# Performance work log

Measured on AMD Instinct MI355X. Metric: run time of the kernel, lower is better.

The kernel has to match this reference:

```python
import jax, jax.numpy as jnp
import numpy as np

B, K, P = 16, 64, 256
D_MODEL, EXPAND = 512, 2
D_INNER = D_MODEL * EXPAND  # 1024
D_CONV, D_FF, E_LAYERS = 4, 16, 4
DT_RANK = 32  # ceil(512/16)
RANK = 4


def rmsnorm(x, w, eps=1e-5):
    return x * jax.lax.rsqrt(jnp.mean(x * x, axis=-1, keepdims=True) + eps) * w


def selective_scan(u, delta, A, Bm, Cm, Dp):
    # u,delta: [b,l,d]; A: [d,n]; Bm,Cm: [b,l,n]; Dp: [d]
    dA = jnp.exp(jnp.einsum('bld,dn->bldn', delta, A))
    dBu = jnp.einsum('bld,bln,bld->bldn', delta, Bm, u)
    x0 = jnp.zeros((u.shape[0], u.shape[2], A.shape[1]), u.dtype)

    def step(x, t):
        dA_t, dBu_t, c_t = t
        x = dA_t * x + dBu_t
        return x, jnp.einsum('bdn,bn->bd', x, c_t)

    _, ys = jax.lax.scan(step, x0, (dA.swapaxes(0, 1), dBu.swapaxes(0, 1), Cm.swapaxes(0, 1)))
    return ys.swapaxes(0, 1) + u * Dp


def mamba_block(h, in_w, cw, cb, xp_w, dt_w, dt_b, A_log, Dp, out_w):
    b, l, _ = h.shape
    xr = h @ in_w.T  # [b,l,2*d_inner]
    x, res = xr[..., :D_INNER], xr[..., D_INNER:]
    # causal depthwise conv1d (torch pads d_conv-1 both sides then trims to l)
    xc = jax.lax.conv_general_dilated(
        x.swapaxes(1, 2), cw, (1,), [(D_CONV - 1, 0)],
        feature_group_count=D_INNER, dimension_numbers=('NCH', 'OIH', 'NCH'))
    x = jax.nn.silu((xc + cb[:, None]).swapaxes(1, 2))
    A = -jnp.exp(A_log)
    x_dbl = x @ xp_w.T
    delta = jax.nn.softplus(x_dbl[..., :DT_RANK] @ dt_w.T + dt_b)
    Bm = x_dbl[..., DT_RANK:DT_RANK + D_FF]
    Cm = x_dbl[..., DT_RANK + D_FF:]
    y = selective_scan(x, delta, A, Bm, Cm, Dp)
    y = y * jax.nn.silu(res)
    return y @ out_w.T


def setup_inputs() -> dict:
    key = jax.random.key(0)
    ks = iter(jax.random.split(key, 32))
    rn = lambda s, sc=0.02: jax.random.normal(next(ks), s, jnp.float32) * sc
    A_init = jnp.log(jnp.tile(jnp.arange(1, D_FF + 1, dtype=jnp.float32)[None, None, :],
                              (E_LAYERS, D_INNER, 1)))
    return {
        'inputs': jax.random.normal(next(ks), (B, K, P), jnp.float32),
        'sp_lin1_w': rn((D_MODEL, P)), 'sp_lin1_b': jnp.zeros((D_MODEL,)),
        'sp_lin2_w': rn((D_MODEL, D_MODEL)), 'sp_lin2_b': jnp.zeros((D_MODEL,)),
        'sp_gate_w': rn((D_MODEL, P)), 'sp_gate_b': jnp.zeros((D_MODEL,)),
        'sp_norm_w': jnp.ones((D_MODEL,)),
        'in_proj_w': rn((E_LAYERS, 2 * D_INNER, D_MODEL)),
        'conv_w': rn((E_LAYERS, D_INNER, 1, D_CONV)),
        'conv_b': jnp.zeros((E_LAYERS, D_INNER)),
        'x_proj_w': rn((E_LAYERS, DT_RANK + 2 * D_FF, D_INNER)),
        'dt_proj_w': rn((E_LAYERS, D_INNER, DT_RANK)),
        'dt_proj_b': jnp.zeros((E_LAYERS, D_INNER)),
        'A_log': A_init,
        'D': jnp.ones((E_LAYERS, D_INNER)),
        'out_proj_w': rn((E_LAYERS, D_MODEL, D_INNER)),
        'blk_norm_w': jnp.ones((E_LAYERS, D_MODEL)),
        'post_norm_w': jnp.ones((D_MODEL,)),
        'proj_w': rn((2 * P * RANK, D_MODEL)),
    }


def reference(inputs, sp_lin1_w, sp_lin1_b, sp_lin2_w, sp_lin2_b, sp_gate_w, sp_gate_b,
              sp_norm_w, in_proj_w, conv_w, conv_b, x_proj_w, dt_proj_w, dt_proj_b,
              A_log, D, out_proj_w, blk_norm_w, post_norm_w, proj_w):
    # SpatialEncoder, shared across lags (pure last-dim linears -> apply to [B,K,P])
    h = jax.nn.gelu(inputs @ sp_lin1_w.T + sp_lin1_b, approximate=False)
    h = h @ sp_lin2_w.T + sp_lin2_b
    g = jax.nn.sigmoid(inputs @ sp_gate_w.T + sp_gate_b)
    h = rmsnorm(h * g, sp_norm_w)  # [B,K,d_model]
    for l in range(E_LAYERS):
        h = mamba_block(rmsnorm(h, blk_norm_w[l]), in_proj_w[l], conv_w[l], conv_b[l],
                        x_proj_w[l], dt_proj_w[l], dt_proj_b[l], A_log[l], D[l],
                        out_proj_w[l]) + h
    h = rmsnorm(h, post_norm_w)
    out = h @ proj_w.T  # [B,K,2*P*RANK]
    U = out[..., :P * RANK].reshape(B, K, P, RANK)
    V = out[..., P * RANK:].reshape(B, K, P, RANK)
    coeffs = jnp.einsum('bkpr,bkqr->bkpq', U, V)
    preds = jnp.einsum('bkpq,bkq->bp', coeffs, inputs)
    return preds, coeffs
```

## Files before the change

kernel.cpp:

```cpp
#include <hip/hip_runtime.h>
#include <hip/hip_bf16.h>
#include <math.h>

namespace {

constexpr int SEQ    = 64;
constexpr int DINNER = 1024;
constexpr int WXPD_STRIDE = 1056 * 1024;

typedef __attribute__((ext_vector_type(8))) short short8;
typedef __attribute__((ext_vector_type(4))) float f32x4;
typedef __attribute__((address_space(3))) unsigned int lds_u32_t;
typedef __attribute__((address_space(1))) unsigned int glb_u32_t;

__device__ __forceinline__ float sigm(float x) { return 1.f / (1.f + __expf(-x)); }
__device__ __forceinline__ short f2b(float v) {
    __hip_bfloat16 h = __float2bfloat16(v);
    return *(short*)&h;
}
__device__ __forceinline__ float b2f(short s) {
    union { unsigned u; float f; } c; c.u = ((unsigned)(unsigned short)s) << 16; return c.f;
}
__device__ __forceinline__ float softp(float v) {
    return fmaxf(v, 0.f) + log1pf(__expf(-fabsf(v)));
}

__device__ __forceinline__ void gemm_core64(
    f32x4 (&acc)[2][2],
    const short* __restrict__ A, int lda,
    const short* __restrict__ W, int ldw,
    int Kd, short* As, short* Bs, int m0, int n0)
{
    constexpr int SZ = 64 * 32;
    const int tid = threadIdx.x, wave = tid >> 6, lane = tid & 63;
    const int wm = wave >> 1, wn = wave & 1;
    const int l15 = lane & 15, kg = lane >> 4;

    const int p = wave * 64 + lane;
    const short* srcA = A + (size_t)(m0 + (p >> 2)) * lda + (p & 3) * 8;
    const short* srcB = W + (size_t)(n0 + (p >> 2)) * ldw + (p & 3) * 8;
    const int ob = (wave * 64) * 8;

    const int nt = Kd >> 5;
    __builtin_amdgcn_global_load_lds((const glb_u32_t*)srcA, (lds_u32_t*)(As + ob), 16, 0, 0);
    __builtin_amdgcn_global_load_lds((const glb_u32_t*)srcB, (lds_u32_t*)(Bs + ob), 16, 0, 0);

    for (int t = 0; t < nt; t++) {
        __syncthreads();
        if (t + 1 < nt) {
            const int k0 = (t + 1) * 32;
            const int s = ((t + 1) & 1) * SZ;
            __builtin_amdgcn_global_load_lds((const glb_u32_t*)(srcA + k0), (lds_u32_t*)(As + s + ob), 16, 0, 0);
            __builtin_amdgcn_global_load_lds((const glb_u32_t*)(srcB + k0), (lds_u32_t*)(Bs + s + ob), 16, 0, 0);
        }
        const short* Ab = As + (t & 1) * SZ;
        const short* Bb = Bs + (t & 1) * SZ;
        short8 af[2], bfr[2];
#pragma unroll
        for (int mi = 0; mi < 2; mi++)
            af[mi] = *(const short8*)(Ab + (wm * 32 + mi * 16 + l15) * 32 + kg * 8);
#pragma unroll
        for (int ni = 0; ni < 2; ni++)
            bfr[ni] = *(const short8*)(Bb + (wn * 32 + ni * 16 + l15) * 32 + kg * 8);
#pragma unroll
        for (int mi = 0; mi < 2; mi++)
#pragma unroll
            for (int ni = 0; ni < 2; ni++)
                acc[mi][ni] = __builtin_amdgcn_mfma_f32_16x16x32_bf16(af[mi], bfr[ni], acc[mi][ni], 0, 0, 0);
    }
}

__global__ __launch_bounds__(256) void prep_k(
    const float* __restrict__ lin1_w, const float* __restrict__ gate_w,
    const float* __restrict__ lin2_w, const float* __restrict__ in_proj_w,
    const float* __restrict__ out_proj_w, const float* __restrict__ proj_w,
    const float* __restrict__ x_proj_w, const float* __restrict__ dt_proj_w,
    const float* __restrict__ inputs, const float* __restrict__ blk_norm_w,
    const float* __restrict__ post_norm_w, const float* __restrict__ sp_norm_w,
    short* __restrict__ wlin1gb, short* __restrict__ wlin2b, short* __restrict__ winpb,
    short* __restrict__ woutpb, short* __restrict__ wprojb, short* __restrict__ wxpdb,
    short* __restrict__ inputsb, float* __restrict__ preds, float* __restrict__ ss)
{
    const int blk = blockIdx.x, tid = threadIdx.x;
    if (blk < 512) {
        const int wave = tid >> 6, lane = tid & 63;
        const int nrow = blk * 8 + wave * 2;
        const int l = nrow >> 10, n = nrow & 1023;
        const float* dtw0 = dt_proj_w + (size_t)l * 32768 + n * 32;
        const float* dtw1 = dtw0 + 32;
        const float* xpw = x_proj_w + (size_t)l * 65536;
        float4 a0[4] = {}, a1[4] = {};
        for (int r = 0; r < 32; r++) {
            const float s0 = dtw0[r], s1 = dtw1[r];
#pragma unroll
            for (int rep = 0; rep < 4; rep++) {
                const float4 xv = *(const float4*)(xpw + r * 1024 + rep * 256 + lane * 4);
                a0[rep].x = fmaf(s0, xv.x, a0[rep].x); a0[rep].y = fmaf(s0, xv.y, a0[rep].y);
                a0[rep].z = fmaf(s0, xv.z, a0[rep].z); a0[rep].w = fmaf(s0, xv.w, a0[rep].w);
                a1[rep].x = fmaf(s1, xv.x, a1[rep].x); a1[rep].y = fmaf(s1, xv.y, a1[rep].y);
                a1[rep].z = fmaf(s1, xv.z, a1[rep].z); a1[rep].w = fmaf(s1, xv.w, a1[rep].w);
            }
        }
        short* dst0 = wxpdb + (size_t)l * WXPD_STRIDE + (size_t)(32 + n) * 1024;
        short* dst1 = dst0 + 1024;
#pragma unroll
        for (int rep = 0; rep < 4; rep++) {
            union { short sh[4]; uint2 u; } p0, p1;
            p0.sh[0] = f2b(a0[rep].x); p0.sh[1] = f2b(a0[rep].y);
            p0.sh[2] = f2b(a0[rep].z); p0.sh[3] = f2b(a0[rep].w);
            p1.sh[0] = f2b(a1[rep].x); p1.sh[1] = f2b(a1[rep].y);
            p1.sh[2] = f2b(a1[rep].z); p1.sh[3] = f2b(a1[rep].w);
            *(uint2*)(dst0 + rep * 256 + lane * 4) = p0.u;
            *(uint2*)(dst1 + rep * 256 + lane * 4) = p1.u;
        }
    } else if (blk < 544) {
#pragma unroll
        for (int rep = 0; rep < 4; rep++) {
            const int idx = (blk - 512) * 4096 + rep * 1024 + tid * 4;
            const int l = idx >> 15, off = idx & 32767;
            const float4 v = *(const float4*)(x_proj_w + (size_t)l * 65536 + 32768 + off);
            union { short sh[4]; uint2 u; } pk;
            pk.sh[0] = f2b(v.x); pk.sh[1] = f2b(v.y); pk.sh[2] = f2b(v.z); pk.sh[3] = f2b(v.w);
            *(uint2*)(wxpdb + (size_t)l * WXPD_STRIDE + off) = pk.u;
        }
    } else if (blk < 1504) {
        constexpr int pre[8] = {0, 128, 256, 512, 4608, 6656, 7680, 7936};
        for (int vb = blk - 544; vb < 7936; vb += 960) {
            int s = 0;
#pragma unroll
            for (int i = 1; i < 7; i++) s += (vb >= pre[i]);
            const int e = (vb - pre[s]) * 1024 + tid * 4;
            const float* src; short* dst;
            bool hasG = false; const float* gp = nullptr;
            bool hasSp = false;
            if      (s == 0) { src = lin1_w + e;     dst = wlin1gb + e; }
            else if (s == 1) { src = gate_w + e;     dst = wlin1gb + 131072 + e; }
            else if (s == 2) { src = lin2_w + e;     dst = wlin2b + e; }
            else if (s == 3) { src = in_proj_w + e;  dst = winpb + e;
                               hasG = true; gp = blk_norm_w + (e >> 20) * 512 + (e & 511);
                               hasSp = ((e >> 20) == 0); }
            else if (s == 4) { src = out_proj_w + e; dst = woutpb + e; }
            else if (s == 5) { src = proj_w + e;     dst = wprojb + e;
                               hasG = true; gp = post_norm_w + (e & 511); }
            else             { src = inputs + e;     dst = inputsb + e; }
            float4 v = *(const float4*)src;
            if (hasG) {
                const float4 gv = *(const float4*)gp;
                v.x *= gv.x; v.y *= gv.y; v.z *= gv.z; v.w *= gv.w;
            }
            if (hasSp) {
                const float4 sv = *(const float4*)(sp_norm_w + (e & 511));
                v.x *= sv.x; v.y *= sv.y; v.z *= sv.z; v.w *= sv.w;
            }
            union { short sh[4]; uint2 u; } pk;
            pk.sh[0] = f2b(v.x); pk.sh[1] = f2b(v.y); pk.sh[2] = f2b(v.z); pk.sh[3] = f2b(v.w);
            *(uint2*)dst = pk.u;
        }
    } else {
        const int i = (blk - 1504) * 256 + tid;
        if (i < 4096) preds[i] = 0.f;
        else ss[i - 4096] = 0.f;
    }
}

__global__ __launch_bounds__(256) void lin1gate_k(
    const short* __restrict__ A, const short* __restrict__ W,
    const float* __restrict__ b1, const float* __restrict__ b2,
    short* __restrict__ h1b, float* __restrict__ g)
{
    __shared__ short As[2 * 64 * 32];
    __shared__ short Bs[2 * 64 * 32];
    f32x4 acc[2][2] = {};
    const int m0 = blockIdx.y * 64, n0 = blockIdx.x * 64;
    gemm_core64(acc, A, 256, W, 256, 256, As, Bs, m0, n0);
    const int lane = threadIdx.x & 63, wave = threadIdx.x >> 6;
    const int wm = wave >> 1, wn = wave & 1, l15 = lane & 15, kg = lane >> 4;
#pragma unroll
    for (int ni = 0; ni < 2; ni++) {
        const int col = n0 + wn * 32 + ni * 16 + l15;
        const bool isG = col >= 512;
        const float b = isG ? b2[col - 512] : b1[col];
#pragma unroll
        for (int mi = 0; mi < 2; mi++)
#pragma unroll
            for (int j = 0; j < 4; j++) {
                const int row = m0 + wm * 32 + mi * 16 + kg * 4 + j;
                const float v = acc[mi][ni][j] + b;
                if (isG) g[(size_t)row * 512 + (col - 512)] = sigm(v);
                else     h1b[(size_t)row * 512 + col] = f2b(0.5f * v * (1.f + erff(v * 0.70710678f)));
            }
    }
}

__global__ __launch_bounds__(256) void lin2_k(
    const short* __restrict__ A, const short* __restrict__ W,
    const float* __restrict__ bias, const float* __restrict__ g,
    const float* __restrict__ gsp, float* __restrict__ x, short* __restrict__ xb,
    float* __restrict__ ssS1, float* __restrict__ ssS2)
{
    __shared__ short As[2 * 64 * 32];
    __shared__ short Bs[2 * 64 * 32];
    f32x4 acc[2][2] = {};
    const int m0 = blockIdx.y * 64, n0 = blockIdx.x * 64;
    gemm_core64(acc, A, 512, W, 512, 512, As, Bs, m0, n0);
    const int lane = threadIdx.x & 63, wave = threadIdx.x >> 6;
    const int wm = wave >> 1, wn = wave & 1, l15 = lane & 15, kg = lane >> 4;
    float vs1[2][4] = {}, vs2[2][4] = {};
#pragma unroll
    for (int ni = 0; ni < 2; ni++) {
        const int col = n0 + wn * 32 + ni * 16 + l15;
        const float b = bias[col];
        const float gc = gsp[col];
#pragma unroll
        for (int mi = 0; mi < 2; mi++)
#pragma unroll
            for (int j = 0; j < 4; j++) {
                const int row = m0 + wm * 32 + mi * 16 + kg * 4 + j;
                const float v = (acc[mi][ni][j] + b) * g[(size_t)row * 512 + col];
                x[(size_t)row * 512 + col] = v;
                xb[(size_t)row * 512 + col] = f2b(v);
                vs1[mi][j] = fmaf(v, v, vs1[mi][j]);
                const float w = v * gc;
                vs2[mi][j] = fmaf(w, w, vs2[mi][j]);
            }
    }
#pragma unroll
    for (int mi = 0; mi < 2; mi++)
#pragma unroll
        for (int j = 0; j < 4; j++) {
            float t1 = vs1[mi][j], t2 = vs2[mi][j];
            t1 += __shfl_xor(t1, 1, 64); t2 += __shfl_xor(t2, 1, 64);
            t1 += __shfl_xor(t1, 2, 64); t2 += __shfl_xor(t2, 2, 64);
            t1 += __shfl_xor(t1, 4, 64); t2 += __shfl_xor(t2, 4, 64);
            t1 += __shfl_xor(t1, 8, 64); t2 += __shfl_xor(t2, 8, 64);
            if (l15 == 0) {
                const int row = m0 + wm * 32 + mi * 16 + kg * 4 + j;
                atomicAdd(ssS1 + row, t1);
                atomicAdd(ssS2 + row, t2);
            }
        }
}

union ConvU {
    struct { short As[2 * 64 * 32]; short Bs[2 * 64 * 32]; } gm;
    float cbuf[67][68];
};

template <int COMB>
__global__ __launch_bounds__(256) void inprojconv_k(
    const short* __restrict__ A, const short* __restrict__ W,
    const float* __restrict__ ssA, const float* __restrict__ ssB,
    const float* __restrict__ cw, const float* __restrict__ cb,
    short* __restrict__ xcb, short* __restrict__ srb)
{
    __shared__ ConvU u;
    f32x4 acc[2][2] = {};
    const int m0 = blockIdx.y * 64, n0 = blockIdx.x * 64;
    gemm_core64(acc, A, 512, W, 512, 512, u.gm.As, u.gm.Bs, m0, n0);
    const int tid = threadIdx.x;
    const int lane = tid & 63, wave = tid >> 6;
    const int wm = wave >> 1, wn = wave & 1, l15 = lane & 15, kg = lane >> 4;

#pragma unroll
    for (int mi = 0; mi < 2; mi++)
#pragma unroll
        for (int j = 0; j < 4; j++) {
            const int row = m0 + wm * 32 + mi * 16 + kg * 4 + j;
            float r;
            if constexpr (COMB) {
                const float rx = rsqrtf(ssA[row] * (1.f / 512.f) + 1e-5f);
                r = rx * rsqrtf(rx * rx * ssB[row] * (1.f / 512.f) + 1e-5f);
            } else {
                r = rsqrtf(ssA[row] * (1.f / 512.f) + 1e-5f);
            }
#pragma unroll
            for (int ni = 0; ni < 2; ni++) acc[mi][ni][j] *= r;
        }

    if (n0 < 1024) {
        const int ccol = tid & 63;
        const int rg = tid >> 6;
        const int d = n0 + ccol;
        const float4 w4 = *(const float4*)(cw + d * 4);
        const float bia = cb[d];

        __syncthreads();
#pragma unroll
        for (int mi = 0; mi < 2; mi++)
#pragma unroll
            for (int ni = 0; ni < 2; ni++)
#pragma unroll
                for (int j = 0; j < 4; j++)
                    u.cbuf[3 + wm * 32 + mi * 16 + kg * 4 + j][wn * 32 + ni * 16 + l15] = acc[mi][ni][j];
        for (int i = tid; i < 3 * 68; i += 256) u.cbuf[i / 68][i % 68] = 0.f;
        __syncthreads();
#pragma unroll 4
        for (int k = 0; k < 16; k++) {
            const int row = rg + 4 * k;
            float v = bia + w4.x * u.cbuf[row][ccol] + w4.y * u.cbuf[row + 1][ccol]
                          + w4.z * u.cbuf[row + 2][ccol] + w4.w * u.cbuf[row + 3][ccol];
            v = v * sigm(v);
            xcb[(size_t)(m0 + row) * 1024 + d] = f2b(v);
        }
    } else {
#pragma unroll
        for (int ni = 0; ni < 2; ni++) {
            const int scol = n0 - 1024 + wn * 32 + ni * 16 + l15;
#pragma unroll
            for (int mi = 0; mi < 2; mi++)
#pragma unroll
                for (int j = 0; j < 4; j++) {
                    const int row = m0 + wm * 32 + mi * 16 + kg * 4 + j;
                    const float v = acc[mi][ni][j];
                    srb[(size_t)row * 1024 + scol] = f2b(v * sigm(v));
                }
        }
    }
}

union XsU {
    struct { short As[2 * 64 * 32]; short Wd[2 * 64 * 32]; short BC[2 * 32 * 32]; } gm;
    struct { float dlt[64][68]; float BC[64][32]; } sc;
};

__global__ __launch_bounds__(256) void xpdscan_k(
    const short* __restrict__ A , const short* __restrict__ W ,
    const float* __restrict__ dtb, const float* __restrict__ Alog,
    const float* __restrict__ Dp, const short* __restrict__ srb, short* __restrict__ yb)
{
    __shared__ XsU u;
    const int dg = blockIdx.x, b = blockIdx.y;
    const int m0 = b * 64;
    const int tid = threadIdx.x;
    const int lane = tid & 63, wave = tid >> 6;
    const int wm = wave >> 1, wn = wave & 1, l15 = lane & 15, kg = lane >> 4;

    constexpr int SZA = 64 * 32, SZBC = 32 * 32;
    const int p = wave * 64 + lane;
    const short* srcA  = A + (size_t)(m0 + (p >> 2)) * 1024 + (p & 3) * 8;
    const short* srcWd = W + (size_t)(32 + dg * 64 + (p >> 2)) * 1024 + (p & 3) * 8;
    const short* srcBC = W + (size_t)(p >> 2) * 1024 + (p & 3) * 8;
    const int ob = (wave * 64) * 8;

    f32x4 accd[2][2] = {};
    f32x4 accx[2] = {};

    __builtin_amdgcn_global_load_lds((const glb_u32_t*)srcA,  (lds_u32_t*)(u.gm.As + ob), 16, 0, 0);
    __builtin_amdgcn_global_load_lds((const glb_u32_t*)srcWd, (lds_u32_t*)(u.gm.Wd + ob), 16, 0, 0);
    if (wave < 2)
        __builtin_amdgcn_global_load_lds((const glb_u32_t*)srcBC, (lds_u32_t*)(u.gm.BC + ob), 16, 0, 0);

    for (int t = 0; t < 32; t++) {
        __syncthreads();
        if (t + 1 < 32) {
            const int k0 = (t + 1) * 32;
            const int sA = ((t + 1) & 1) * SZA, sBC = ((t + 1) & 1) * SZBC;
            __builtin_amdgcn_global_load_lds((const glb_u32_t*)(srcA + k0),  (lds_u32_t*)(u.gm.As + sA + ob), 16, 0, 0);
            __builtin_amdgcn_global_load_lds((const glb_u32_t*)(srcWd + k0), (lds_u32_t*)(u.gm.Wd + sA + ob), 16, 0, 0);
            if (wave < 2)
                __builtin_amdgcn_global_load_lds((const glb_u32_t*)(srcBC + k0), (lds_u32_t*)(u.gm.BC + sBC + ob), 16, 0, 0);
        }
        const short* Ab  = u.gm.As + (t & 1) * SZA;
        const short* Wdb = u.gm.Wd + (t & 1) * SZA;
        const short* BCb = u.gm.BC + (t & 1) * SZBC;
        short8 af[2], wf[2], bcf;
#pragma unroll
        for (int mi = 0; mi < 2; mi++)
            af[mi] = *(const short8*)(Ab + (wm * 32 + mi * 16 + l15) * 32 + kg * 8);
#pragma unroll
        for (int ni = 0; ni < 2; ni++)
            wf[ni] = *(const short8*)(Wdb + (wn * 32 + ni * 16 + l15) * 32 + kg * 8);
        bcf = *(const short8*)(BCb + (wn * 16 + l15) * 32 + kg * 8);
#pragma unroll
        for (int mi = 0; mi < 2; mi++) {
#pragma unroll
            for (int ni = 0; ni < 2; ni++)
                accd[mi][ni] = __builtin_amdgcn_mfma_f32_16x16x32_bf16(af[mi], wf[ni], accd[mi][ni], 0, 0, 0);
            accx[mi] = __builtin_amdgcn_mfma_f32_16x16x32_bf16(af[mi], bcf, accx[mi], 0, 0, 0);
        }
    }

    __syncthreads();
#pragma unroll
    for (int ni = 0; ni < 2; ni++) {
        const int dl = wn * 32 + ni * 16 + l15;
        const float bb = dtb[dg * 64 + dl];
#pragma unroll
        for (int mi = 0; mi < 2; mi++)
#pragma unroll
            for (int j = 0; j < 4; j++)
                u.sc.dlt[wm * 32 + mi * 16 + kg * 4 + j][dl] = softp(accd[mi][ni][j] + bb);
    }
    {
        const int c = wn * 16 + l15;
#pragma unroll
        for (int mi = 0; mi < 2; mi++)
#pragma unroll
            for (int j = 0; j < 4; j++)
                u.sc.BC[wm * 32 + mi * 16 + kg * 4 + j][c] = accx[mi][j];
    }
    __syncthreads();

    {
        const int d_l = tid >> 2;
        const int ns = (tid & 3) << 2;
        const int d = dg * 64 + d_l;
        float a[4], s[4];
#pragma unroll
        for (int n = 0; n < 4; n++) {
            a[n] = -__expf(Alog[(size_t)d * 16 + ns + n]);
            s[n] = 0.f;
        }
        const float dv = Dp[d];
        const size_t base = (size_t)b * SEQ;
        float uu = b2f(A[base * DINNER + d]);
        float rr = b2f(srb[base * 1024 + d]);
        for (int l = 0; l < SEQ; l++) {
            float uu_n = 0.f, rr_n = 0.f;
            if (l + 1 < SEQ) {
                uu_n = b2f(A[(base + l + 1) * DINNER + d]);
                rr_n = b2f(srb[(base + l + 1) * 1024 + d]);
            }
            const float dlt = u.sc.dlt[l][d_l];
            const float dbu = dlt * uu;
            float part = 0.f;
#pragma unroll
            for (int n = 0; n < 4; n++) {
                s[n] = __expf(dlt * a[n]) * s[n] + dbu * u.sc.BC[l][ns + n];
                part = fmaf(s[n], u.sc.BC[l][16 + ns + n], part);
            }
            part += __shfl_xor(part, 1, 64);
            part += __shfl_xor(part, 2, 64);
            if ((tid & 3) == 0)
                yb[(base + l) * DINNER + d] = f2b((part + uu * dv) * rr);
            uu = uu_n; rr = rr_n;
        }
    }
}

template <int FIRST>
__global__ __launch_bounds__(256) void outproj_k(
    const short* __restrict__ A, const short* __restrict__ W,
    float* __restrict__ h, short* __restrict__ hb, float* __restrict__ ss_out,
    const float* __restrict__ xsrc, const float* __restrict__ gsp,
    const float* __restrict__ ssS1)
{
    __shared__ short As[2 * 32 * 32];
    __shared__ short Bs[2 * 64 * 32];
    constexpr int SZA = 32 * 32, SZB = 64 * 32;
    const int m0 = blockIdx.y * 32, n0 = blockIdx.x * 64;
    const int tid = threadIdx.x, wave = tid >> 6, lane = tid & 63;
    const int l15 = lane & 15, kg = lane >> 4;

    const int p = wave * 64 + lane;
    const short* srcA = A + (size_t)(m0 + (p >> 2)) * 1024 + (p & 3) * 8;
    const short* srcB = W + (size_t)(n0 + (p >> 2)) * 1024 + (p & 3) * 8;
    const int ob = (wave * 64) * 8;

    f32x4 acc[2] = {};
    if (wave < 2)
        __builtin_amdgcn_global_load_lds((const glb_u32_t*)srcA, (lds_u32_t*)(As + ob), 16, 0, 0);
    __builtin_amdgcn_global_load_lds((const glb_u32_t*)srcB, (lds_u32_t*)(Bs + ob), 16, 0, 0);

    for (int t = 0; t < 32; t++) {
        __syncthreads();
        if (t + 1 < 32) {
            const int k0 = (t + 1) * 32;
            const int sA = ((t + 1) & 1) * SZA, sB = ((t + 1) & 1) * SZB;
            if (wave < 2)
                __builtin_amdgcn_global_load_lds((const glb_u32_t*)(srcA + k0), (lds_u32_t*)(As + sA + ob), 16, 0, 0);
            __builtin_amdgcn_global_load_lds((const glb_u32_t*)(srcB + k0), (lds_u32_t*)(Bs + sB + ob), 16, 0, 0);
        }
        const short* Ab = As + (t & 1) * SZA;
        const short* Bb = Bs + (t & 1) * SZB;
        short8 af[2], bf;
#pragma unroll
        for (int mi = 0; mi < 2; mi++)
            af[mi] = *(const short8*)(Ab + (mi * 16 + l15) * 32 + kg * 8);
        bf = *(const short8*)(Bb + (wave * 16 + l15) * 32 + kg * 8);
#pragma unroll
        for (int mi = 0; mi < 2; mi++)
            acc[mi] = __builtin_amdgcn_mfma_f32_16x16x32_bf16(af[mi], bf, acc[mi], 0, 0, 0);
    }

    const int col = n0 + wave * 16 + l15;
    const float gc = FIRST ? gsp[col] : 0.f;
    float vsq[2][4] = {};
#pragma unroll
    for (int mi = 0; mi < 2; mi++)
#pragma unroll
        for (int j = 0; j < 4; j++) {
            const int row = m0 + mi * 16 + kg * 4 + j;
            float hold;
            if constexpr (FIRST) {
                const float rx = rsqrtf(ssS1[row] * (1.f / 512.f) + 1e-5f);
                hold = xsrc[(size_t)row * 512 + col] * rx * gc;
            } else {
                hold = h[(size_t)row * 512 + col];
            }
            const float v = acc[mi][j] + hold;
            h[(size_t)row * 512 + col] = v;
            hb[(size_t)row * 512 + col] = f2b(v);
            vsq[mi][j] = v * v;
        }
#pragma unroll
    for (int mi = 0; mi < 2; mi++)
#pragma unroll
        for (int j = 0; j < 4; j++) {
            float t = vsq[mi][j];
            t += __shfl_xor(t, 1, 64);
            t += __shfl_xor(t, 2, 64);
            t += __shfl_xor(t, 4, 64);
            t += __shfl_xor(t, 8, 64);
            if (l15 == 0) {
                const int row = m0 + mi * 16 + kg * 4 + j;
                atomicAdd(ss_out + row, t);
            }
        }
}

__global__ __launch_bounds__(256) void projf_k(
    const short* __restrict__ A, const short* __restrict__ W,
    const float* __restrict__ ss_in, float* __restrict__ xr)
{
    __shared__ short As[2 * 64 * 32];
    __shared__ short Bs[2 * 64 * 32];
    f32x4 acc[2][2] = {};
    const int m0 = blockIdx.y * 64, n0 = blockIdx.x * 64;
    gemm_core64(acc, A, 512, W, 512, 512, As, Bs, m0, n0);
    const int lane = threadIdx.x & 63, wave = threadIdx.x >> 6;
    const int wm = wave >> 1, wn = wave & 1, l15 = lane & 15, kg = lane >> 4;
#pragma unroll
    for (int mi = 0; mi < 2; mi++)
#pragma unroll
        for (int j = 0; j < 4; j++) {
            const int row = m0 + wm * 32 + mi * 16 + kg * 4 + j;
            const float r = rsqrtf(ss_in[row] * (1.f / 512.f) + 1e-5f);
#pragma unroll
            for (int ni = 0; ni < 2; ni++) {
                const int col = n0 + wn * 32 + ni * 16 + l15;
                xr[(size_t)row * 2048 + col] = acc[mi][ni][j] * r;
            }
        }
}

__global__ __launch_bounds__(256) void coeffs_k(
    const float* __restrict__ outp, const float* __restrict__ inp,
    float* __restrict__ coeffs, float* __restrict__ preds)
{
    const int m = blockIdx.x;
    const int b = m >> 6;
    const int tid = threadIdx.x, wave = tid >> 6, lane = tid & 63;
    __shared__ float4 Us[256], Vs[256];
    __shared__ float ins[256];
    __shared__ float4 tpart[4];
    Us[tid] = *(const float4*)(outp + (size_t)m * 2048 + tid * 4);
    Vs[tid] = *(const float4*)(outp + (size_t)m * 2048 + 1024 + tid * 4);
    ins[tid] = inp[(size_t)m * 256 + tid];
    __syncthreads();
    const float4 vq0 = Vs[lane * 4 + 0], vq1 = Vs[lane * 4 + 1];
    const float4 vq2 = Vs[lane * 4 + 2], vq3 = Vs[lane * 4 + 3];
    float* cbase = coeffs + (size_t)m * 65536 + lane * 4;
#pragma unroll 4
    for (int i = 0; i < 64; i++) {
        const int pp = (wave << 6) + i;
        const float4 up = Us[pp];
        float4 c;
        c.x = up.x * vq0.x + up.y * vq0.y + up.z * vq0.z + up.w * vq0.w;
        c.y = up.x * vq1.x + up.y * vq1.y + up.z * vq1.z + up.w * vq1.w;
        c.z = up.x * vq2.x + up.y * vq2.y + up.z * vq2.z + up.w * vq2.w;
        c.w = up.x * vq3.x + up.y * vq3.y + up.z * vq3.z + up.w * vq3.w;
        *(float4*)(cbase + (size_t)pp * 256) = c;
    }
    const float iv = ins[tid];
    const float4 vm = Vs[tid];
    float4 t = make_float4(vm.x * iv, vm.y * iv, vm.z * iv, vm.w * iv);
#pragma unroll
    for (int off = 32; off > 0; off >>= 1) {
        t.x += __shfl_xor(t.x, off, 64);
        t.y += __shfl_xor(t.y, off, 64);
        t.z += __shfl_xor(t.z, off, 64);
        t.w += __shfl_xor(t.w, off, 64);
    }
    if (lane == 0) tpart[wave] = t;
    __syncthreads();
    const float4 t0 = tpart[0], t1 = tpart[1], t2 = tpart[2], t3 = tpart[3];
    const float4 tt = make_float4(t0.x + t1.x + t2.x + t3.x, t0.y + t1.y + t2.y + t3.y,
                                  t0.z + t1.z + t2.z + t3.z, t0.w + t1.w + t2.w + t3.w);
    const float4 up = Us[tid];
    const float pv = up.x * tt.x + up.y * tt.y + up.z * tt.z + up.w * tt.w;
    atomicAdd(preds + (size_t)b * 256 + tid, pv);
}

}

extern "C" void kernel_launch(void* const* d_in, const int* in_sizes, int n_in,
                              void* d_out, int out_size, void* d_ws, size_t ws_size,
                              hipStream_t stream)
{
    const float* inputs     = (const float*)d_in[0];
    const float* lin1_w     = (const float*)d_in[1];
    const float* lin1_b     = (const float*)d_in[2];
    const float* lin2_w     = (const float*)d_in[3];
    const float* lin2_b     = (const float*)d_in[4];
    const float* gate_w     = (const float*)d_in[5];
    const float* gate_b     = (const float*)d_in[6];
    const float* sp_norm_w  = (const float*)d_in[7];
    const float* in_proj_w  = (const float*)d_in[8];
    const float* conv_w     = (const float*)d_in[9];
    const float* conv_b     = (const float*)d_in[10];
    const float* x_proj_w   = (const float*)d_in[11];
    const float* dt_proj_w  = (const float*)d_in[12];
    const float* dt_proj_b  = (const float*)d_in[13];
    const float* A_log      = (const float*)d_in[14];
    const float* Dvec       = (const float*)d_in[15];
    const float* out_proj_w = (const float*)d_in[16];
    const float* blk_norm_w = (const float*)d_in[17];
    const float* post_norm_w= (const float*)d_in[18];
    const float* proj_w     = (const float*)d_in[19];

    float* ws = (float*)d_ws;
    float* h     = ws;
    float* xr    = ws + 524288;
    float* x     = ws + 2621440;
    float* g     = ws + 3145728;
    float* ss    = ws + 3670016;
    short* bfb     = (short*)(ws + 3676160);
    short* inputsb = bfb;
    short* h1b     = bfb + 262144;
    short* hb      = bfb + 786432;
    short* xcb     = bfb + 1310720;
    short* yb      = bfb + 2359296;
    short* xb      = yb;
    short* srb     = bfb + 3407872;
    short* wlin1gb = bfb + 4456448;
    short* wlin2b  = bfb + 4718592;
    short* winpb   = bfb + 4980736;
    short* woutpb  = bfb + 9175040;
    short* wprojb  = bfb + 11272192;
    short* wxpdb   = bfb + 12320768;
    float* preds  = (float*)d_out;
    float* coeffs = (float*)d_out + 4096;

    const dim3 blk(256);

    prep_k<<<dim3(1544), blk, 0, stream>>>(
        lin1_w, gate_w, lin2_w, in_proj_w, out_proj_w, proj_w, x_proj_w, dt_proj_w,
        inputs, blk_norm_w, post_norm_w, sp_norm_w,
        wlin1gb, wlin2b, winpb, woutpb, wprojb, wxpdb, inputsb, preds, ss);

    lin1gate_k<<<dim3(16, 16), blk, 0, stream>>>(inputsb, wlin1gb, lin1_b, gate_b, h1b, g);
    lin2_k<<<dim3(8, 16), blk, 0, stream>>>(h1b, wlin2b, lin2_b, g, sp_norm_w,
                                            x, xb, ss, ss + 5120);

    for (int l = 0; l < 4; l++) {
        if (l == 0)
            inprojconv_k<1><<<dim3(32, 16), blk, 0, stream>>>(
                xb, winpb, ss, ss + 5120,
                conv_w, conv_b, xcb, srb);
        else
            inprojconv_k<0><<<dim3(32, 16), blk, 0, stream>>>(
                hb, winpb + (size_t)l * 1048576, ss + l * 1024, nullptr,
                conv_w + (size_t)l * 4096, conv_b + l * 1024, xcb, srb);
        xpdscan_k<<<dim3(16, 16), blk, 0, stream>>>(
            xcb, wxpdb + (size_t)l * WXPD_STRIDE, dt_proj_b + l * 1024,
            A_log + (size_t)l * 16384, Dvec + l * 1024, srb, yb);
        if (l == 0)
            outproj_k<1><<<dim3(8, 32), blk, 0, stream>>>(yb, woutpb,
                h, hb, ss + 1024, x, sp_norm_w, ss);
        else
            outproj_k<0><<<dim3(8, 32), blk, 0, stream>>>(yb, woutpb + (size_t)l * 524288,
                h, hb, ss + (l + 1) * 1024, nullptr, nullptr, nullptr);
    }

    projf_k<<<dim3(32, 16), blk, 0, stream>>>(hb, wprojb, ss + 4096, xr);
    coeffs_k<<<dim3(1024), blk, 0, stream>>>(xr, inputs, coeffs, preds);
}
```

Before: 404.0 us.

## Widen GEMM K-tile to 64 with XOR-swizzled LDS and stage scan I/O through LDS

The shared 64x64 GEMM core now loads a 64-wide K slice per stage instead of 32, with an XOR swizzle on the LDS layout to avoid bank conflicts. This halves the number of barrier and pipeline iterations but doubles LDS per block. Separately, the selective-scan kernel stages its u input and its y output in LDS and uses coalesced 16-byte vector loads and stores for u, the gate and y. This replaces strided per-element global accesses inside the sequential loop. The cost is more LDS use, which could reduce occupancy.

```diff
diff --git a/kernel.cpp b/kernel.cpp
--- a/kernel.cpp
+++ b/kernel.cpp
@@ -31,42 +31,59 @@
     const short* __restrict__ W, int ldw,
     int Kd, short* As, short* Bs, int m0, int n0)
 {
-    constexpr int SZ = 64 * 32;
+    constexpr int SZ = 64 * 64;
     const int tid = threadIdx.x, wave = tid >> 6, lane = tid & 63;
     const int wm = wave >> 1, wn = wave & 1;
     const int l15 = lane & 15, kg = lane >> 4;
 
-    const int p = wave * 64 + lane;
-    const short* srcA = A + (size_t)(m0 + (p >> 2)) * lda + (p & 3) * 8;
-    const short* srcB = W + (size_t)(n0 + (p >> 2)) * ldw + (p & 3) * 8;
-    const int ob = (wave * 64) * 8;
-
-    const int nt = Kd >> 5;
-    __builtin_amdgcn_global_load_lds((const glb_u32_t*)srcA, (lds_u32_t*)(As + ob), 16, 0, 0);
-    __builtin_amdgcn_global_load_lds((const glb_u32_t*)srcB, (lds_u32_t*)(Bs + ob), 16, 0, 0);
+    const int r0 = tid >> 3,        s0 = tid & 7;
+    const int r1 = 32 + (tid >> 3), s1 = s0;
+    const short* srcA0 = A + (size_t)(m0 + r0) * lda + ((s0 ^ (r0 & 7)) * 8);
+    const short* srcA1 = A + (size_t)(m0 + r1) * lda + ((s1 ^ (r1 & 7)) * 8);
+    const short* srcB0 = W + (size_t)(n0 + r0) * ldw + ((s0 ^ (r0 & 7)) * 8);
+    const short* srcB1 = W + (size_t)(n0 + r1) * ldw + ((s1 ^ (r1 & 7)) * 8);
+    const int ob0 = wave * 512;
+    const int ob1 = 2048 + wave * 512;
+
+    const int nt = Kd >> 6;
+    __builtin_amdgcn_global_load_lds((const glb_u32_t*)srcA0, (lds_u32_t*)(As + ob0), 16, 0, 0);
+    __builtin_amdgcn_global_load_lds((const glb_u32_t*)srcA1, (lds_u32_t*)(As + ob1), 16, 0, 0);
+    __builtin_amdgcn_global_load_lds((const glb_u32_t*)srcB0, (lds_u32_t*)(Bs + ob0), 16, 0, 0);
+    __builtin_amdgcn_global_load_lds((const glb_u32_t*)srcB1, (lds_u32_t*)(Bs + ob1), 16, 0, 0);
 
     for (int t = 0; t < nt; t++) {
         __syncthreads();
         if (t + 1 < nt) {
-            const int k0 = (t + 1) * 32;
+            const int k0 = (t + 1) * 64;
             const int s = ((t + 1) & 1) * SZ;
-            __builtin_amdgcn_global_load_lds((const glb_u32_t*)(srcA + k0), (lds_u32_t*)(As + s + ob), 16, 0, 0);
-            __builtin_amdgcn_global_load_lds((const glb_u32_t*)(srcB + k0), (lds_u32_t*)(Bs + s + ob), 16, 0, 0);
+            __builtin_amdgcn_global_load_lds((const glb_u32_t*)(srcA0 + k0), (lds_u32_t*)(As + s + ob0), 16, 0, 0);
+            __builtin_amdgcn_global_load_lds((const glb_u32_t*)(srcA1 + k0), (lds_u32_t*)(As + s + ob1), 16, 0, 0);
+            __builtin_amdgcn_global_load_lds((const glb_u32_t*)(srcB0 + k0), (lds_u32_t*)(Bs + s + ob0), 16, 0, 0);
+            __builtin_amdgcn_global_load_lds((const glb_u32_t*)(srcB1 + k0), (lds_u32_t*)(Bs + s + ob1), 16, 0, 0);
         }
         const short* Ab = As + (t & 1) * SZ;
         const short* Bb = Bs + (t & 1) * SZ;
-        short8 af[2], bfr[2];
-#pragma unroll
-        for (int mi = 0; mi < 2; mi++)
-            af[mi] = *(const short8*)(Ab + (wm * 32 + mi * 16 + l15) * 32 + kg * 8);
-#pragma unroll
-        for (int ni = 0; ni < 2; ni++)
-            bfr[ni] = *(const short8*)(Bb + (wn * 32 + ni * 16 + l15) * 32 + kg * 8);
-#pragma unroll
-        for (int mi = 0; mi < 2; mi++)
-#pragma unroll
-            for (int ni = 0; ni < 2; ni++)
-                acc[mi][ni] = __builtin_amdgcn_mfma_f32_16x16x32_bf16(af[mi], bfr[ni], acc[mi][ni], 0, 0, 0);
+        short8 af[2][2], bfr[2][2];
+#pragma unroll
+        for (int hk = 0; hk < 2; hk++) {
+#pragma unroll
+            for (int mi = 0; mi < 2; mi++) {
+                const int row = wm * 32 + mi * 16 + l15;
+                af[hk][mi] = *(const short8*)(Ab + row * 64 + (((hk * 4 + kg) ^ (row & 7)) * 8));
+            }
+#pragma unroll
+            for (int ni = 0; ni < 2; ni++) {
+                const int row = wn * 32 + ni * 16 + l15;
+                bfr[hk][ni] = *(const short8*)(Bb + row * 64 + (((hk * 4 + kg) ^ (row & 7)) * 8));
+            }
+        }
+#pragma unroll
+        for (int hk = 0; hk < 2; hk++)
+#pragma unroll
+            for (int mi = 0; mi < 2; mi++)
+#pragma unroll
+                for (int ni = 0; ni < 2; ni++)
+                    acc[mi][ni] = __builtin_amdgcn_mfma_f32_16x16x32_bf16(af[hk][mi], bfr[hk][ni], acc[mi][ni], 0, 0, 0);
     }
 }
 
@@ -168,8 +185,8 @@
     const float* __restrict__ b1, const float* __restrict__ b2,
     short* __restrict__ h1b, float* __restrict__ g)
 {
-    __shared__ short As[2 * 64 * 32];
-    __shared__ short Bs[2 * 64 * 32];
+    __shared__ short As[2 * 64 * 64];
+    __shared__ short Bs[2 * 64 * 64];
     f32x4 acc[2][2] = {};
     const int m0 = blockIdx.y * 64, n0 = blockIdx.x * 64;
     gemm_core64(acc, A, 256, W, 256, 256, As, Bs, m0, n0);
@@ -198,8 +215,8 @@
     const float* __restrict__ gsp, float* __restrict__ x, short* __restrict__ xb,
     float* __restrict__ ssS1, float* __restrict__ ssS2)
 {
-    __shared__ short As[2 * 64 * 32];
-    __shared__ short Bs[2 * 64 * 32];
+    __shared__ short As[2 * 64 * 64];
+    __shared__ short Bs[2 * 64 * 64];
     f32x4 acc[2][2] = {};
     const int m0 = blockIdx.y * 64, n0 = blockIdx.x * 64;
     gemm_core64(acc, A, 512, W, 512, 512, As, Bs, m0, n0);
@@ -242,7 +259,7 @@
 }
 
 union ConvU {
-    struct { short As[2 * 64 * 32]; short Bs[2 * 64 * 32]; } gm;
+    struct { short As[2 * 64 * 64]; short Bs[2 * 64 * 64]; } gm;
     float cbuf[67][68];
 };
 
@@ -320,7 +337,7 @@
 
 union XsU {
     struct { short As[2 * 64 * 32]; short Wd[2 * 64 * 32]; short BC[2 * 32 * 32]; } gm;
-    struct { float dlt[64][68]; float BC[64][32]; } sc;
+    struct { float dlt[64][68]; float BC[64][32]; short ub[64][64]; float yt[64][68]; } sc;
 };
 
 __global__ __launch_bounds__(256) void xpdscan_k(
@@ -399,6 +416,13 @@
             for (int j = 0; j < 4; j++)
                 u.sc.BC[wm * 32 + mi * 16 + kg * 4 + j][c] = accx[mi][j];
     }
+#pragma unroll
+    for (int k = 0; k < 2; k++) {
+        const int c = tid + k * 256;
+        const int row = c >> 3, sl = c & 7;
+        *(uint4*)&u.sc.ub[row][sl * 8] =
+            *(const uint4*)(A + (size_t)(m0 + row) * 1024 + dg * 64 + sl * 8);
+    }
     __syncthreads();
 
     {
@@ -412,16 +436,9 @@
             s[n] = 0.f;
         }
         const float dv = Dp[d];
-        const size_t base = (size_t)b * SEQ;
-        float uu = b2f(A[base * DINNER + d]);
-        float rr = b2f(srb[base * 1024 + d]);
         for (int l = 0; l < SEQ; l++) {
-            float uu_n = 0.f, rr_n = 0.f;
-            if (l + 1 < SEQ) {
-                uu_n = b2f(A[(base + l + 1) * DINNER + d]);
-                rr_n = b2f(srb[(base + l + 1) * 1024 + d]);
-            }
             const float dlt = u.sc.dlt[l][d_l];
+            const float uu = b2f(u.sc.ub[l][d_l]);
             const float dbu = dlt * uu;
             float part = 0.f;
 #pragma unroll
@@ -431,10 +448,20 @@
             }
             part += __shfl_xor(part, 1, 64);
             part += __shfl_xor(part, 2, 64);
-            if ((tid & 3) == 0)
-                yb[(base + l) * DINNER + d] = f2b((part + uu * dv) * rr);
-            uu = uu_n; rr = rr_n;
-        }
+            if ((tid & 3) == 0) u.sc.yt[l][d_l] = part + uu * dv;
+        }
+    }
+    __syncthreads();
+#pragma unroll
+    for (int k = 0; k < 2; k++) {
+        const int c = tid + k * 256;
+        const int row = c >> 3, sl = c & 7;
+        const short8 rv = *(const short8*)(srb + (size_t)(m0 + row) * 1024 + dg * 64 + sl * 8);
+        short8 out;
+#pragma unroll
+        for (int j = 0; j < 8; j++)
+            out[j] = f2b(u.sc.yt[row][sl * 8 + j] * b2f(rv[j]));
+        *(short8*)(yb + (size_t)(m0 + row) * 1024 + dg * 64 + sl * 8) = out;
     }
 }
 
@@ -523,8 +550,8 @@
     const short* __restrict__ A, const short* __restrict__ W,
     const float* __restrict__ ss_in, float* __restrict__ xr)
 {
-    __shared__ short As[2 * 64 * 32];
-    __shared__ short Bs[2 * 64 * 32];
+    __shared__ short As[2 * 64 * 64];
+    __shared__ short Bs[2 * 64 * 64];
     f32x4 acc[2][2] = {};
     const int m0 = blockIdx.y * 64, n0 = blockIdx.x * 64;
     gemm_core64(acc, A, 512, W, 512, 512, As, Bs, m0, n0);
```

After: 375.2 us. 1.08x faster.
